# Optimization experiments

Measured on AMD Instinct MI355X. Metric: run time of the kernel, lower is better.

The kernel has to match this reference:

```python
import jax, jax.numpy as jnp
import numpy as np

H = 6144  # canvas_shape[0]
W = 6144  # canvas_shape[1]
LINE_WIDTH = 1.0


def setup_inputs() -> dict:
    key = jax.random.key(0)
    k0, k1 = jax.random.split(key)
    p0 = jax.random.uniform(k0, (2,), dtype=jnp.float32)
    p1 = jax.random.uniform(k1, (2,), dtype=jnp.float32)
    return {"p0": p0, "p1": p1}


def reference(p0, p1):
    # Scale normalized endpoints to pixel coordinates (same as torch.tensor(canvas_shape) mult).
    shape_vec = jnp.array([H, W], dtype=jnp.float32)
    p0 = p0 * shape_vec
    p1 = p1 * shape_vec
    d = p1 - p0                              # p1_minus_p0, shape [2]
    len_sq = d[0] ** 2 + d[1] ** 2           # squared segment length (scalar)

    # Original loops: canvas[x, y] evaluated at point p = (x, y).
    # x indexes the first canvas axis, y the second (square canvas).
    X = jnp.arange(H, dtype=jnp.float32)[:, None]   # [H, 1] -> p_x
    Y = jnp.arange(W, dtype=jnp.float32)[None, :]   # [1, W] -> p_y

    px = X - p0[0]                           # (p - p0)_x, broadcasts to [H, W]
    py = Y - p0[1]
    t = jnp.clip((px * d[0] + py * d[1]) / len_sq, 0.0, 1.0)  # [H, W]
    proj_x = p0[0] + t * d[0]
    proj_y = p0[1] + t * d[1]
    dist = jnp.sqrt((X - proj_x) ** 2 + (Y - proj_y) ** 2)    # [H, W]

    canvas = jnp.where(dist < LINE_WIDTH, LINE_WIDTH - dist, jnp.float32(0.0))
    return canvas
```

## Files before the change

kernel.cpp:

```cpp
#include <hip/hip_runtime.h>

#define CANVAS_H 6144
#define CANVAS_W 6144
#define LINE_WIDTH 1.0f
#define PIX_PER_THREAD 4
#define BLOCK 256

__global__ __launch_bounds__(BLOCK) void
LineRaster2d_kernel(const float* __restrict__ p0g,
                    const float* __restrict__ p1g,
                    float* __restrict__ out) {
    const long long tid  = (long long)blockIdx.x * BLOCK + threadIdx.x;
    const long long base = tid * PIX_PER_THREAD;

    const int x  = (int)(base / CANVAS_W);
    const int y0 = (int)(base % CANVAS_W);

    const float p0x = p0g[0] * (float)CANVAS_H;
    const float p0y = p0g[1] * (float)CANVAS_W;
    const float p1x = p1g[0] * (float)CANVAS_H;
    const float p1y = p1g[1] * (float)CANVAS_W;
    const float dx = p1x - p0x;
    const float dy = p1y - p0y;
    const float inv_len_sq = 1.0f / (dx * dx + dy * dy);

    const float px = (float)x - p0x;
    const float px_dx = px * dx;

    float4 r;
    float* rp = &r.x;
#pragma unroll
    for (int j = 0; j < PIX_PER_THREAD; ++j) {
        const float py = (float)(y0 + j) - p0y;
        float t = (px_dx + py * dy) * inv_len_sq;
        t = fminf(fmaxf(t, 0.0f), 1.0f);
        const float ex = px - t * dx;
        const float ey = py - t * dy;
        const float dist = sqrtf(ex * ex + ey * ey);
        rp[j] = (dist < LINE_WIDTH) ? (LINE_WIDTH - dist) : 0.0f;
    }

    *reinterpret_cast<float4*>(out + base) = r;
}

extern "C" void kernel_launch(void* const* d_in, const int* in_sizes, int n_in,
                              void* d_out, int out_size, void* d_ws, size_t ws_size,
                              hipStream_t stream) {
    const float* p0 = (const float*)d_in[0];
    const float* p1 = (const float*)d_in[1];
    float* out = (float*)d_out;

    const long long n_pix = (long long)CANVAS_H * CANVAS_W;
    const int n_blocks = (int)(n_pix / (PIX_PER_THREAD * BLOCK));

    LineRaster2d_kernel<<<n_blocks, BLOCK, 0, stream>>>(p0, p1, out);
}
```

Before: 155.8 us.

## Use persistent row-striped blocks with cheap far-from-line test and nontemporal stores

Replaces the one-shot 4-pixel-per-thread grid with 1536 persistent blocks of 384 threads, each looping over rows and writing 16 pixels per thread per row. A conservative squared-distance test at each 4-pixel group centre lets groups far from the segment write zeros without the full per-pixel evaluation. Output goes through nontemporal vector stores, and the reciprocal and square root use fast hardware builtins. The kernel is bound by writes to a 150 MB canvas, so the compute savings may matter little, while the fast intrinsics can introduce small precision differences.

```diff
diff --git a/kernel.cpp b/kernel.cpp
--- a/kernel.cpp
+++ b/kernel.cpp
@@ -1,46 +1,66 @@
 #include <hip/hip_runtime.h>
 
-#define CANVAS_H 6144
-#define CANVAS_W 6144
-#define LINE_WIDTH 1.0f
-#define PIX_PER_THREAD 4
-#define BLOCK 256
+#define H 6144
+#define W 6144
+#define BLOCK 384
+#define GRID  1536
+#define GSTRIDE 1536
+
+typedef float v4f __attribute__((ext_vector_type(4)));
 
 __global__ __launch_bounds__(BLOCK) void
 LineRaster2d_kernel(const float* __restrict__ p0g,
                     const float* __restrict__ p1g,
                     float* __restrict__ out) {
-    const long long tid  = (long long)blockIdx.x * BLOCK + threadIdx.x;
-    const long long base = tid * PIX_PER_THREAD;
+    const float p0x = p0g[0] * (float)H;
+    const float p0y = p0g[1] * (float)W;
+    const float dx  = p1g[0] * (float)H - p0x;
+    const float dy  = p1g[1] * (float)W - p0y;
+    const float inv_len_sq = __builtin_amdgcn_rcpf(dx * dx + dy * dy);
 
-    const int x  = (int)(base / CANVAS_W);
-    const int y0 = (int)(base % CANVAS_W);
+    const int   t       = threadIdx.x;
+    const float py_base = (float)(t * 4) - p0y;
 
-    const float p0x = p0g[0] * (float)CANVAS_H;
-    const float p0y = p0g[1] * (float)CANVAS_W;
-    const float p1x = p1g[0] * (float)CANVAS_H;
-    const float p1y = p1g[1] * (float)CANVAS_W;
-    const float dx = p1x - p0x;
-    const float dy = p1y - p0y;
-    const float inv_len_sq = 1.0f / (dx * dx + dy * dy);
+    for (int r = blockIdx.x; r < H; r += GRID) {
+        const float px    = (float)r - p0x;
+        const float px_dx = px * dx;
+        v4f* row4 = reinterpret_cast<v4f*>(out + (size_t)r * W) + t;
 
-    const float px = (float)x - p0x;
-    const float px_dx = px * dx;
+        float d2[4];
+#pragma unroll
+        for (int j = 0; j < 4; ++j) {
+            const float pyc = py_base + (float)(j * GSTRIDE) + 1.5f;
+            float tc = (px_dx + pyc * dy) * inv_len_sq;
+            tc = fminf(fmaxf(tc, 0.0f), 1.0f);
+            const float ex = px  - tc * dx;
+            const float ey = pyc - tc * dy;
+            d2[j] = ex * ex + ey * ey;
+        }
+        const float d2min = fminf(fminf(d2[0], d2[1]), fminf(d2[2], d2[3]));
 
-    float4 r;
-    float* rp = &r.x;
+        if (d2min < 9.0f) {
 #pragma unroll
-    for (int j = 0; j < PIX_PER_THREAD; ++j) {
-        const float py = (float)(y0 + j) - p0y;
-        float t = (px_dx + py * dy) * inv_len_sq;
-        t = fminf(fmaxf(t, 0.0f), 1.0f);
-        const float ex = px - t * dx;
-        const float ey = py - t * dy;
-        const float dist = sqrtf(ex * ex + ey * ey);
-        rp[j] = (dist < LINE_WIDTH) ? (LINE_WIDTH - dist) : 0.0f;
+            for (int j = 0; j < 4; ++j) {
+                v4f v = (v4f)0.0f;
+#pragma unroll
+                for (int i = 0; i < 4; ++i) {
+                    const float py = py_base + (float)(j * GSTRIDE + i);
+                    float tt = (px_dx + py * dy) * inv_len_sq;
+                    tt = fminf(fmaxf(tt, 0.0f), 1.0f);
+                    const float ex = px - tt * dx;
+                    const float ey = py - tt * dy;
+                    const float dist = __builtin_amdgcn_sqrtf(ex * ex + ey * ey);
+                    v[i] = (dist < 1.0f) ? (1.0f - dist) : 0.0f;
+                }
+                __builtin_nontemporal_store(v, row4 + j * (GSTRIDE / 4));
+            }
+        } else {
+            const v4f z = (v4f)0.0f;
+#pragma unroll
+            for (int j = 0; j < 4; ++j)
+                __builtin_nontemporal_store(z, row4 + j * (GSTRIDE / 4));
+        }
     }
-
-    *reinterpret_cast<float4*>(out + base) = r;
 }
 
 extern "C" void kernel_launch(void* const* d_in, const int* in_sizes, int n_in,
@@ -50,8 +70,5 @@
     const float* p1 = (const float*)d_in[1];
     float* out = (float*)d_out;
 
-    const long long n_pix = (long long)CANVAS_H * CANVAS_W;
-    const int n_blocks = (int)(n_pix / (PIX_PER_THREAD * BLOCK));
-
-    LineRaster2d_kernel<<<n_blocks, BLOCK, 0, stream>>>(p0, p1, out);
+    LineRaster2d_kernel<<<GRID, BLOCK, 0, stream>>>(p0, p1, out);
 }
```

Measured after the change: 159.4 us. +2.3%, slower.

## Rasterize only pixels near the line after zero-filling the canvas

Applied to the files above, without the earlier changes.

Replaces the dense per-pixel evaluation with a hipMemsetAsync zero-fill of the whole canvas followed by a sparse kernel. The sparse kernel walks the line's major axis and evaluates an 8-pixel window around the line centre at each step, writing only pixels whose distance is below one. This removes the sqrt/projection arithmetic for almost all pixels and leaves a memset-bound fill. It also switches to approximate rcp/sqrt intrinsics, which may change results slightly. The window may miss pixels near the segment endpoints or for degenerate segments.

```diff
diff --git a/kernel.cpp b/kernel.cpp
--- a/kernel.cpp
+++ b/kernel.cpp
@@ -1,46 +1,57 @@
 #include <hip/hip_runtime.h>
 
-#define CANVAS_H 6144
-#define CANVAS_W 6144
-#define LINE_WIDTH 1.0f
-#define PIX_PER_THREAD 4
+#define H 6144
+#define W 6144
 #define BLOCK 256
+#define MAJOR_SLOTS 6176
+#define GRID ((MAJOR_SLOTS * 8) / BLOCK)
 
 __global__ __launch_bounds__(BLOCK) void
-LineRaster2d_kernel(const float* __restrict__ p0g,
+LineRaster2d_sparse(const float* __restrict__ p0g,
                     const float* __restrict__ p1g,
                     float* __restrict__ out) {
-    const long long tid  = (long long)blockIdx.x * BLOCK + threadIdx.x;
-    const long long base = tid * PIX_PER_THREAD;
+    const int i     = blockIdx.x * BLOCK + threadIdx.x;
+    const int m_idx = i >> 3;
+    const int off   = i & 7;
 
-    const int x  = (int)(base / CANVAS_W);
-    const int y0 = (int)(base % CANVAS_W);
+    const float p0x = p0g[0] * (float)H;
+    const float p0y = p0g[1] * (float)W;
+    const float p1x = p1g[0] * (float)H;
+    const float p1y = p1g[1] * (float)W;
+    const float dx  = p1x - p0x;
+    const float dy  = p1y - p0y;
+    const float inv_len_sq = __builtin_amdgcn_rcpf(dx * dx + dy * dy);
 
-    const float p0x = p0g[0] * (float)CANVAS_H;
-    const float p0y = p0g[1] * (float)CANVAS_W;
-    const float p1x = p1g[0] * (float)CANVAS_H;
-    const float p1y = p1g[1] * (float)CANVAS_W;
-    const float dx = p1x - p0x;
-    const float dy = p1y - p0y;
-    const float inv_len_sq = 1.0f / (dx * dx + dy * dy);
+    const bool xmajor = fabsf(dx) >= fabsf(dy);
+    const float pm0 = xmajor ? p0x : p0y;
+    const float pm1 = xmajor ? p1x : p1y;
+    const float pn0 = xmajor ? p0y : p0x;
+    const float dm  = pm1 - pm0;
+    const float dn  = xmajor ? dy : dx;
+    const float inv_dm = (dm != 0.0f) ? __builtin_amdgcn_rcpf(dm) : 0.0f;
+
+    const int m = (int)floorf(fminf(pm0, pm1)) - 2 + m_idx;
+    if ((unsigned)m >= (unsigned)H) return;
+
+    float ct = ((float)m - pm0) * inv_dm;
+    ct = fminf(fmaxf(ct, 0.0f), 1.0f);
+    const float center = pn0 + ct * dn;
+
+    const int n = (int)floorf(center) - 3 + off;
+    if ((unsigned)n >= (unsigned)W) return;
+
+    const int x = xmajor ? m : n;
+    const int y = xmajor ? n : m;
 
     const float px = (float)x - p0x;
-    const float px_dx = px * dx;
+    const float py = (float)y - p0y;
+    float t = (px * dx + py * dy) * inv_len_sq;
+    t = fminf(fmaxf(t, 0.0f), 1.0f);
+    const float ex = px - t * dx;
+    const float ey = py - t * dy;
+    const float dist = __builtin_amdgcn_sqrtf(ex * ex + ey * ey);
 
-    float4 r;
-    float* rp = &r.x;
-#pragma unroll
-    for (int j = 0; j < PIX_PER_THREAD; ++j) {
-        const float py = (float)(y0 + j) - p0y;
-        float t = (px_dx + py * dy) * inv_len_sq;
-        t = fminf(fmaxf(t, 0.0f), 1.0f);
-        const float ex = px - t * dx;
-        const float ey = py - t * dy;
-        const float dist = sqrtf(ex * ex + ey * ey);
-        rp[j] = (dist < LINE_WIDTH) ? (LINE_WIDTH - dist) : 0.0f;
-    }
-
-    *reinterpret_cast<float4*>(out + base) = r;
+    if (dist < 1.0f) out[(size_t)x * W + y] = 1.0f - dist;
 }
 
 extern "C" void kernel_launch(void* const* d_in, const int* in_sizes, int n_in,
@@ -50,8 +61,6 @@
     const float* p1 = (const float*)d_in[1];
     float* out = (float*)d_out;
 
-    const long long n_pix = (long long)CANVAS_H * CANVAS_W;
-    const int n_blocks = (int)(n_pix / (PIX_PER_THREAD * BLOCK));
-
-    LineRaster2d_kernel<<<n_blocks, BLOCK, 0, stream>>>(p0, p1, out);
+    hipMemsetAsync(out, 0, (size_t)out_size * sizeof(float), stream);
+    LineRaster2d_sparse<<<GRID, BLOCK, 0, stream>>>(p0, p1, out);
 }
```

Result: faster. 151.2 us (-2.9%).
